# Kernel optimization log

Hardware: AMD Instinct MI355X
Metric: run time of the kernel (lower is better)

Reference implementation:

```python
import jax, jax.numpy as jnp
import numpy as np

N, C, H, M = 4096, 1024, 16, 4096
D = C // H
EPS = 1e-6


def rms_norm(x, g):
    # RMSNorm32: normalize in fp32 with eps=1e-6, affine scale g
    x32 = x.astype(jnp.float32)
    inv = jax.lax.rsqrt(jnp.mean(x32 * x32, axis=-1, keepdims=True) + EPS)
    return (x32 * inv).astype(x.dtype) * g


def setup_inputs() -> dict:
    key = jax.random.key(0)
    ks = jax.random.split(key, 6)
    s = 1.0 / np.sqrt(C)
    return {
        "x": jax.random.normal(ks[0], (N, C), jnp.float32),
        "g1": jnp.ones((C,), jnp.float32),
        "g2": jnp.ones((C,), jnp.float32),
        "w_qkv": jax.random.normal(ks[1], (C, 3 * C), jnp.float32) * s,
        "w_o": jax.random.normal(ks[2], (C, C), jnp.float32) * s,
        "w1": jax.random.normal(ks[3], (C, M), jnp.float32) * s,
        "w2": jax.random.normal(ks[4], (M, C), jnp.float32) * (1.0 / np.sqrt(M)),
    }


def reference(x, g1, g2, w_qkv, w_o, w1, w2):
    # --- pre-norm + full multi-head self-attention over all N sparse tokens ---
    h = rms_norm(x, g1)                                   # [N, C]
    qkv = (h @ w_qkv).reshape(N, 3, H, D)                 # [N, 3, H, D]
    q, k, v = qkv[:, 0], qkv[:, 1], qkv[:, 2]             # [N, H, D]
    scale = 1.0 / np.sqrt(D)
    scores = jnp.einsum('nhd,mhd->hnm', q, k) * scale     # [H, N, N]
    attn = jax.nn.softmax(scores, axis=-1)
    o = jnp.einsum('hnm,mhd->nhd', attn, v).reshape(N, C) # [N, C]
    x = x + o @ w_o                                       # residual
    # --- pre-norm + gated-free MLP (GELU tanh) ---
    h2 = rms_norm(x, g2)
    m = jax.nn.gelu(h2 @ w1, approximate=True) @ w2       # [N, C]
    return x + m
```

## Files before the change

kernel.cpp:

```cpp
#include <hip/hip_runtime.h>
#include <stdint.h>

#define TOK 4096
#define CH  1024
#define NH  16
#define HD  64
#define FF  4096

typedef __attribute__((ext_vector_type(8))) short bf16x8;
typedef __attribute__((ext_vector_type(4))) float f32x4;
typedef __attribute__((ext_vector_type(16))) float f32x16;

__device__ __forceinline__ unsigned short f2bf(float f) {
    union { float f; unsigned u; } v; v.f = f;
    unsigned u = v.u;
    u += 0x7fffu + ((u >> 16) & 1u);
    return (unsigned short)(u >> 16);
}

__device__ __forceinline__ unsigned cvtpk(float a, float b) {
    unsigned r;
    asm("v_cvt_pk_bf16_f32 %0, %1, %2" : "=v"(r) : "v"(a), "v"(b));
    return r;
}

__device__ __forceinline__ void load_lds16(const void* g, void* l) {
    __builtin_amdgcn_global_load_lds(
        (const __attribute__((address_space(1))) unsigned int*)g,
        (__attribute__((address_space(3))) unsigned int*)l, 16, 0, 0);
}

template<int N> __device__ __forceinline__ void wait_vm_lgkm0() {
    if constexpr (N == 0)      asm volatile("s_waitcnt vmcnt(0) lgkmcnt(0)" ::: "memory");
    else if constexpr (N == 4) asm volatile("s_waitcnt vmcnt(4) lgkmcnt(0)" ::: "memory");
    __builtin_amdgcn_sched_barrier(0);
    __builtin_amdgcn_s_barrier();
}

__device__ __forceinline__ float gelu_tanh(float u) {
    float z = 0.7978845608028654f * (u + 0.044715f * u * u * u);
    float e = __expf(2.0f * z);
    return 0.5f * u * (1.0f + (1.0f - 2.0f / (e + 1.0f)));
}

__global__ __launch_bounds__(256) void wT_kernel(const float* __restrict__ in,
                                                 unsigned short* __restrict__ out,
                                                 int K, int Nn) {
    __shared__ float tile[32][33];
    int k0 = blockIdx.x * 32, n0 = blockIdx.y * 32;
    int t = threadIdx.x, r = t >> 3, c = t & 7;
#pragma unroll
    for (int i = 0; i < 4; i++)
        tile[r][c + 8 * i] = in[(size_t)(k0 + r) * Nn + n0 + c + 8 * i];
    __syncthreads();
#pragma unroll
    for (int i = 0; i < 4; i++)
        out[(size_t)(n0 + r) * K + k0 + c + 8 * i] = f2bf(tile[c + 8 * i][r]);
}

__global__ __launch_bounds__(256) void rms_kernel(const float* __restrict__ x,
                                                  const float* __restrict__ g,
                                                  unsigned short* __restrict__ out) {
    int row = blockIdx.x, t = threadIdx.x;
    const float4* xr = (const float4*)(x + (size_t)row * CH);
    float4 v = xr[t];
    float ss = v.x * v.x + v.y * v.y + v.z * v.z + v.w * v.w;
#pragma unroll
    for (int m = 32; m; m >>= 1) ss += __shfl_xor(ss, m, 64);
    __shared__ float wsum[4];
    if ((t & 63) == 0) wsum[t >> 6] = ss;
    __syncthreads();
    float inv = rsqrtf((wsum[0] + wsum[1] + wsum[2] + wsum[3]) * (1.0f / CH) + 1e-6f);
    float4 gv = ((const float4*)g)[t];
    ushort4 o;
    o.x = f2bf(v.x * inv * gv.x);
    o.y = f2bf(v.y * inv * gv.y);
    o.z = f2bf(v.z * inv * gv.z);
    o.w = f2bf(v.w * inv * gv.w);
    ((ushort4*)(out + (size_t)row * CH))[t] = o;
}

template<int BM, int BN, int EPI>
__global__ __launch_bounds__(256) void gemm_bt(const unsigned short* __restrict__ A,
                                               const unsigned short* __restrict__ Bt,
                                               void* __restrict__ outp,
                                               const float* __restrict__ resid,
                                               unsigned short* __restrict__ vout,
                                               int M, int Nn, int K) {
    __shared__ __align__(16) unsigned short ldsA[2][BM * 32];
    __shared__ __align__(16) unsigned short ldsB[2][BN * 32];
    const int t = threadIdx.x, l = t & 63, w = t >> 6;
    const int nbn = Nn / BN;
    const int bid = blockIdx.x, nwg = gridDim.x, cpx = nwg >> 3;
    const int swz = (bid & 7) * cpx + (bid >> 3);
    const int bm = swz / nbn, bn = swz % nbn;
    const int wr = w >> 1, wc = w & 1;
    constexpr int MF = BM / 32, NF = BN / 32;
    const unsigned short* Ag = A + (size_t)bm * BM * K;
    const unsigned short* Bg = Bt + (size_t)bn * BN * K;

    f32x4 acc[MF][NF];
#pragma unroll
    for (int m = 0; m < MF; m++)
#pragma unroll
        for (int n = 0; n < NF; n++) acc[m][n] = {0.f, 0.f, 0.f, 0.f};

    auto stage = [&](int buf, int kt) {
#pragma unroll
        for (int p = 0; p < BM / 64; p++) {
            int c = t + 256 * p;
            load_lds16(Ag + (size_t)(c >> 2) * K + kt * 32 + (c & 3) * 8, &ldsA[buf][c * 8]);
        }
#pragma unroll
        for (int p = 0; p < BN / 64; p++) {
            int c = t + 256 * p;
            load_lds16(Bg + (size_t)(c >> 2) * K + kt * 32 + (c & 3) * 8, &ldsB[buf][c * 8]);
        }
    };

    stage(0, 0);
    __syncthreads();
    const int nkt = K >> 5;
    for (int kt = 0; kt < nkt; kt++) {
        const int buf = kt & 1;
        if (kt + 1 < nkt) stage(buf ^ 1, kt + 1);
        bf16x8 af[MF], bfr[NF];
#pragma unroll
        for (int m = 0; m < MF; m++)
            af[m] = *(const bf16x8*)&ldsA[buf][(wr * (BM / 2) + m * 16 + (l & 15)) * 32 + (l >> 4) * 8];
#pragma unroll
        for (int n = 0; n < NF; n++)
            bfr[n] = *(const bf16x8*)&ldsB[buf][(wc * (BN / 2) + n * 16 + (l & 15)) * 32 + (l >> 4) * 8];
#pragma unroll
        for (int m = 0; m < MF; m++)
#pragma unroll
            for (int n = 0; n < NF; n++)
                acc[m][n] = __builtin_amdgcn_mfma_f32_16x16x32_bf16(af[m], bfr[n], acc[m][n], 0, 0, 0);
        __syncthreads();
    }

    const int r0 = bm * BM + wr * (BM / 2), c0 = bn * BN + wc * (BN / 2);
    const bool vpart = (EPI == 3) && (c0 >= 2048);
#pragma unroll
    for (int m = 0; m < MF; m++)
#pragma unroll
        for (int n = 0; n < NF; n++) {
            if (vpart) {
                int cc = c0 + n * 16 + (l & 15);
                int rrb = r0 + m * 16 + (l >> 4) * 4;
                ushort4 pk;
                pk.x = f2bf(acc[m][n][0]);
                pk.y = f2bf(acc[m][n][1]);
                pk.z = f2bf(acc[m][n][2]);
                pk.w = f2bf(acc[m][n][3]);
                *(ushort4*)(vout + (size_t)(cc - 2048) * 4096 + rrb) = pk;
            } else {
#pragma unroll
                for (int r = 0; r < 4; r++) {
                    int rr = r0 + m * 16 + (l >> 4) * 4 + r;
                    int cc = c0 + n * 16 + (l & 15);
                    float v = acc[m][n][r];
                    if (EPI == 0) {
                        ((unsigned short*)outp)[(size_t)rr * Nn + cc] = f2bf(v);
                    } else if (EPI == 1) {
                        ((unsigned short*)outp)[(size_t)rr * Nn + cc] = f2bf(gelu_tanh(v));
                    } else if (EPI == 3) {
                        float sc = (cc < 1024) ? 0.180336880f : 1.0f;
                        ((unsigned short*)outp)[(size_t)rr * Nn + cc] = f2bf(v * sc);
                    } else {
                        ((float*)outp)[(size_t)rr * Nn + cc] = resid[(size_t)rr * Nn + cc] + v;
                    }
                }
            }
        }
}

__global__ __launch_bounds__(256) void attn_kernel(const unsigned short* __restrict__ qkv,
                                                   const unsigned short* __restrict__ vT,
                                                   unsigned short* __restrict__ o) {
    __shared__ __align__(16) unsigned short Kl[3][4096];
    __shared__ __align__(16) unsigned short Vl[3][4096];
    const int t = threadIdx.x, l = t & 63, w = t >> 6;
    const int h = blockIdx.y;
    const int qrow = blockIdx.x * 128 + w * 32 + (l & 31);

    bf16x8 qf[4];
    {
        const unsigned short* qp = qkv + (size_t)qrow * 3072 + h * 64 + ((l >> 5) * 8);
#pragma unroll
        for (int c = 0; c < 4; c++) qf[c] = *(const bf16x8*)(qp + 16 * c);
    }
    const unsigned short* kb = qkv + 1024 + h * 64;
    const unsigned short* vb = vT + (size_t)h * 64 * 4096;

    int off8[4];
#pragma unroll
    for (int c = 0; c < 4; c++)
        off8[c] = (l & 31) * 64 + ((((l >> 5) + 2 * c) ^ (l & 7)) * 8);
    int kst[2], vst[2];
#pragma unroll
    for (int p = 0; p < 2; p++) {
        int c = t + 256 * p;
        int r = c >> 3, b = c & 7;
        kst[p] = r * 3072 + ((b ^ (r & 7)) * 8);
        vst[p] = r * 4096 + ((b ^ (r & 7)) * 8);
    }

    float lrun = 0.f;
    const f32x16 z16 = {0.f, 0.f, 0.f, 0.f, 0.f, 0.f, 0.f, 0.f,
                        0.f, 0.f, 0.f, 0.f, 0.f, 0.f, 0.f, 0.f};
    f32x16 accO[2];
#pragma unroll
    for (int dt = 0; dt < 2; dt++) accO[dt] = z16;

    auto stage = [&](int buf, int kt) {
#pragma unroll
        for (int p = 0; p < 2; p++)
            load_lds16(kb + (size_t)kt * 64 * 3072 + kst[p], &Kl[buf][(t + 256 * p) * 8]);
#pragma unroll
        for (int p = 0; p < 2; p++)
            load_lds16(vb + kt * 64 + vst[p], &Vl[buf][(t + 256 * p) * 8]);
    };

    stage(0, 0);
    stage(1, 1);
    wait_vm_lgkm0<4>();

    for (int kt = 0; kt < 64; kt++) {
        const int cur = kt % 3;
        if (kt + 2 < 64) stage((kt + 2) % 3, kt + 2);

        f32x16 s[2];
        __builtin_amdgcn_s_setprio(1);
#pragma unroll
        for (int st = 0; st < 2; st++) {
            bf16x8 kf0 = *(const bf16x8*)&Kl[cur][st * 2048 + off8[0]];
            s[st] = __builtin_amdgcn_mfma_f32_32x32x16_bf16(kf0, qf[0], z16, 0, 0, 0);
#pragma unroll
            for (int c = 1; c < 4; c++) {
                bf16x8 kf = *(const bf16x8*)&Kl[cur][st * 2048 + off8[c]];
                s[st] = __builtin_amdgcn_mfma_f32_32x32x16_bf16(kf, qf[c], s[st], 0, 0, 0);
            }
        }
        __builtin_amdgcn_s_setprio(0);

        float rs = 0.f;
#pragma unroll
        for (int st = 0; st < 2; st++)
#pragma unroll
            for (int i = 0; i < 16; i++) {
                float p = __builtin_amdgcn_exp2f(s[st][i]);
                s[st][i] = p;
                rs += p;
            }
        lrun += rs;

#pragma unroll
        for (int kc = 0; kc < 4; kc++) {
            const int base = 8 * (kc & 1);
            const f32x16& S = s[kc >> 1];
            unsigned w0 = cvtpk(S[base + 0], S[base + 1]);
            unsigned w1 = cvtpk(S[base + 2], S[base + 3]);
            unsigned w2 = cvtpk(S[base + 4], S[base + 5]);
            unsigned w3 = cvtpk(S[base + 6], S[base + 7]);
            asm("v_permlane32_swap_b32 %0, %1" : "+v"(w0), "+v"(w2));
            asm("v_permlane32_swap_b32 %0, %1" : "+v"(w1), "+v"(w3));
            union { unsigned u[4]; bf16x8 v; } pf;
            pf.u[0] = w0; pf.u[1] = w1; pf.u[2] = w2; pf.u[3] = w3;
            __builtin_amdgcn_s_setprio(1);
#pragma unroll
            for (int dt = 0; dt < 2; dt++) {
                bf16x8 vf = *(const bf16x8*)&Vl[cur][dt * 2048 + off8[kc]];
                accO[dt] = __builtin_amdgcn_mfma_f32_32x32x16_bf16(vf, pf.v, accO[dt], 0, 0, 0);
            }
            __builtin_amdgcn_s_setprio(0);
        }

        if (kt < 63) {
            if (kt + 2 < 64) wait_vm_lgkm0<4>();
            else             wait_vm_lgkm0<0>();
        }
    }

    lrun += __shfl_xor(lrun, 32, 64);
    float inv = 1.0f / lrun;
    unsigned short* ob = o + (size_t)qrow * CH + h * 64 + 4 * (l >> 5);
#pragma unroll
    for (int dt = 0; dt < 2; dt++)
#pragma unroll
        for (int qd = 0; qd < 4; qd++) {
            ushort4 pk;
            pk.x = f2bf(accO[dt][qd * 4 + 0] * inv);
            pk.y = f2bf(accO[dt][qd * 4 + 1] * inv);
            pk.z = f2bf(accO[dt][qd * 4 + 2] * inv);
            pk.w = f2bf(accO[dt][qd * 4 + 3] * inv);
            *(ushort4*)(ob + dt * 32 + qd * 8) = pk;
        }
}

extern "C" void kernel_launch(void* const* d_in, const int* in_sizes, int n_in,
                              void* d_out, int out_size, void* d_ws, size_t ws_size,
                              hipStream_t stream) {
    const float* x     = (const float*)d_in[0];
    const float* g1    = (const float*)d_in[1];
    const float* g2    = (const float*)d_in[2];
    const float* w_qkv = (const float*)d_in[3];
    const float* w_o   = (const float*)d_in[4];
    const float* w1    = (const float*)d_in[5];
    const float* w2    = (const float*)d_in[6];

    char* ws = (char*)d_ws;
    unsigned short* wqkvT = (unsigned short*)(ws);
    unsigned short* woT   = (unsigned short*)(ws + 6291456);
    unsigned short* w1T   = (unsigned short*)(ws + 8388608);
    unsigned short* w2T   = (unsigned short*)(ws + 16777216);
    unsigned short* hbuf  = (unsigned short*)(ws + 25165824);
    unsigned short* qkv   = (unsigned short*)(ws + 33554432);
    unsigned short* obuf  = (unsigned short*)(ws + 58720256);
    float*          x2    = (float*)(ws + 67108864);
    unsigned short* abuf  = (unsigned short*)(ws + 83886080);
    unsigned short* vTb   = (unsigned short*)(ws + 83886080);

    dim3 b256(256);
    wT_kernel<<<dim3(CH / 32, 3 * CH / 32), b256, 0, stream>>>(w_qkv, wqkvT, CH, 3 * CH);
    wT_kernel<<<dim3(CH / 32, CH / 32),     b256, 0, stream>>>(w_o,   woT,   CH, CH);
    wT_kernel<<<dim3(CH / 32, FF / 32),     b256, 0, stream>>>(w1,    w1T,   CH, FF);
    wT_kernel<<<dim3(FF / 32, CH / 32),     b256, 0, stream>>>(w2,    w2T,   FF, CH);

    rms_kernel<<<TOK, b256, 0, stream>>>(x, g1, hbuf);
    gemm_bt<128, 128, 3><<<(TOK / 128) * (3 * CH / 128), b256, 0, stream>>>(hbuf, wqkvT, qkv, nullptr, vTb, TOK, 3 * CH, CH);
    attn_kernel<<<dim3(TOK / 128, NH), b256, 0, stream>>>(qkv, vTb, obuf);
    gemm_bt<64, 64, 2><<<(TOK / 64) * (CH / 64), b256, 0, stream>>>(obuf, woT, x2, x, nullptr, TOK, CH, CH);
    rms_kernel<<<TOK, b256, 0, stream>>>(x2, g2, hbuf);
    gemm_bt<128, 128, 1><<<(TOK / 128) * (FF / 128), b256, 0, stream>>>(hbuf, w1T, abuf, nullptr, nullptr, TOK, FF, CH);
    gemm_bt<64, 64, 2><<<(TOK / 64) * (CH / 64), b256, 0, stream>>>(abuf, w2T, (float*)d_out, x2, nullptr, TOK, CH, FF);
}
```

Before: 305.8 us.

## Software-pipeline attention loop with 4-deep K/V buffers and QK lookahead

Restructures the attention main loop so the QK^T MFMAs for the next key tile are issued before the softmax and PV work of the current tile, using two alternating score register sets. K/V LDS staging grows from triple to quadruple buffering, prefetching three tiles ahead with adjusted vmcnt waits. The goal is to hide exp/convert latency and load latency behind matrix work. In exchange it raises LDS use per block to 64KB, which may lower the number of resident blocks, and it increases register pressure.

After: 307.5 us. No clear change (+0.6%).

```diff
diff --git a/kernel.cpp b/kernel.cpp
--- a/kernel.cpp
+++ b/kernel.cpp
@@ -33,6 +33,7 @@
 template<int N> __device__ __forceinline__ void wait_vm_lgkm0() {
     if constexpr (N == 0)      asm volatile("s_waitcnt vmcnt(0) lgkmcnt(0)" ::: "memory");
     else if constexpr (N == 4) asm volatile("s_waitcnt vmcnt(4) lgkmcnt(0)" ::: "memory");
+    else if constexpr (N == 8) asm volatile("s_waitcnt vmcnt(8) lgkmcnt(0)" ::: "memory");
     __builtin_amdgcn_sched_barrier(0);
     __builtin_amdgcn_s_barrier();
 }
@@ -178,8 +179,8 @@
 __global__ __launch_bounds__(256) void attn_kernel(const unsigned short* __restrict__ qkv,
                                                    const unsigned short* __restrict__ vT,
                                                    unsigned short* __restrict__ o) {
-    __shared__ __align__(16) unsigned short Kl[3][4096];
-    __shared__ __align__(16) unsigned short Vl[3][4096];
+    __shared__ __align__(16) unsigned short Kl[4][4096];
+    __shared__ __align__(16) unsigned short Vl[4][4096];
     const int t = threadIdx.x, l = t & 63, w = t >> 6;
     const int h = blockIdx.y;
     const int qrow = blockIdx.x * 128 + w * 32 + (l & 31);
@@ -213,37 +214,33 @@
 #pragma unroll
     for (int dt = 0; dt < 2; dt++) accO[dt] = z16;
 
-    auto stage = [&](int buf, int kt) {
+    auto stage = [&](int tile) {
+        const int buf = tile & 3;
 #pragma unroll
         for (int p = 0; p < 2; p++)
-            load_lds16(kb + (size_t)kt * 64 * 3072 + kst[p], &Kl[buf][(t + 256 * p) * 8]);
+            load_lds16(kb + (size_t)tile * 64 * 3072 + kst[p], &Kl[buf][(t + 256 * p) * 8]);
 #pragma unroll
         for (int p = 0; p < 2; p++)
-            load_lds16(vb + kt * 64 + vst[p], &Vl[buf][(t + 256 * p) * 8]);
+            load_lds16(vb + tile * 64 + vst[p], &Vl[buf][(t + 256 * p) * 8]);
     };
 
-    stage(0, 0);
-    stage(1, 1);
-    wait_vm_lgkm0<4>();
-
-    for (int kt = 0; kt < 64; kt++) {
-        const int cur = kt % 3;
-        if (kt + 2 < 64) stage((kt + 2) % 3, kt + 2);
-
-        f32x16 s[2];
+    auto qk = [&](int tile, f32x16* s) {
+        const unsigned short* kl = &Kl[tile & 3][0];
         __builtin_amdgcn_s_setprio(1);
 #pragma unroll
         for (int st = 0; st < 2; st++) {
-            bf16x8 kf0 = *(const bf16x8*)&Kl[cur][st * 2048 + off8[0]];
+            bf16x8 kf0 = *(const bf16x8*)&kl[st * 2048 + off8[0]];
             s[st] = __builtin_amdgcn_mfma_f32_32x32x16_bf16(kf0, qf[0], z16, 0, 0, 0);
 #pragma unroll
             for (int c = 1; c < 4; c++) {
-                bf16x8 kf = *(const bf16x8*)&Kl[cur][st * 2048 + off8[c]];
+                bf16x8 kf = *(const bf16x8*)&kl[st * 2048 + off8[c]];
                 s[st] = __builtin_amdgcn_mfma_f32_32x32x16_bf16(kf, qf[c], s[st], 0, 0, 0);
             }
         }
         __builtin_amdgcn_s_setprio(0);
-
+    };
+
+    auto smpv = [&](int tile, f32x16* s) {
         float rs = 0.f;
 #pragma unroll
         for (int st = 0; st < 2; st++)
@@ -254,7 +251,7 @@
                 rs += p;
             }
         lrun += rs;
-
+        const unsigned short* vl = &Vl[tile & 3][0];
 #pragma unroll
         for (int kc = 0; kc < 4; kc++) {
             const int base = 8 * (kc & 1);
@@ -270,15 +267,33 @@
             __builtin_amdgcn_s_setprio(1);
 #pragma unroll
             for (int dt = 0; dt < 2; dt++) {
-                bf16x8 vf = *(const bf16x8*)&Vl[cur][dt * 2048 + off8[kc]];
+                bf16x8 vf = *(const bf16x8*)&vl[dt * 2048 + off8[kc]];
                 accO[dt] = __builtin_amdgcn_mfma_f32_32x32x16_bf16(vf, pf.v, accO[dt], 0, 0, 0);
             }
             __builtin_amdgcn_s_setprio(0);
         }
-
-        if (kt < 63) {
-            if (kt + 2 < 64) wait_vm_lgkm0<4>();
-            else             wait_vm_lgkm0<0>();
+    };
+
+    f32x16 sA[2], sB[2];
+
+    stage(0); stage(1); stage(2);
+    wait_vm_lgkm0<8>();
+    qk(0, sA);
+
+    for (int j = 0; j < 64; j += 2) {
+        if (j <= 60) wait_vm_lgkm0<4>();
+        else         wait_vm_lgkm0<0>();
+        if (j + 3 < 64) stage(j + 3);
+        qk(j + 1, sB);
+        smpv(j, sA);
+        const int jo = j + 1;
+        if (jo < 63) {
+            wait_vm_lgkm0<4>();
+            if (jo + 3 < 64) stage(jo + 3);
+            qk(jo + 1, sA);
+            smpv(jo, sB);
+        } else {
+            smpv(63, sB);
         }
     }
 
```

## Add 256x256-tile 512-thread GEMM for QKV and FC1 projections

Applied to the files above, without the earlier changes.

Introduces a new gemm256 kernel with 256x256 output tiles, 8 waves, 64-wide K steps, XOR-swizzled LDS layout, quarter-step staging interleaved with MFMA compute, and s_setprio around the MFMA bursts. The QKV projection (with its V-transpose epilogue) and the FC1+GELU projection now use it instead of the 128x128 gemm_bt. The aim is higher arithmetic intensity per LDS byte and better overlap of global-to-LDS loads with compute. In exchange it uses more registers and LDS, and it launches fewer workgroups (192 and 256), which may leave the GPU's CUs under-occupied.

New measurement: 293.7 us. -4.0%, faster.

```diff
diff --git a/kernel.cpp b/kernel.cpp
--- a/kernel.cpp
+++ b/kernel.cpp
@@ -33,6 +33,7 @@
 template<int N> __device__ __forceinline__ void wait_vm_lgkm0() {
     if constexpr (N == 0)      asm volatile("s_waitcnt vmcnt(0) lgkmcnt(0)" ::: "memory");
     else if constexpr (N == 4) asm volatile("s_waitcnt vmcnt(4) lgkmcnt(0)" ::: "memory");
+    else if constexpr (N == 8) asm volatile("s_waitcnt vmcnt(8) lgkmcnt(0)" ::: "memory");
     __builtin_amdgcn_sched_barrier(0);
     __builtin_amdgcn_s_barrier();
 }
@@ -85,7 +86,6 @@
                                                const unsigned short* __restrict__ Bt,
                                                void* __restrict__ outp,
                                                const float* __restrict__ resid,
-                                               unsigned short* __restrict__ vout,
                                                int M, int Nn, int K) {
     __shared__ __align__(16) unsigned short ldsA[2][BM * 32];
     __shared__ __align__(16) unsigned short ldsB[2][BN * 32];
@@ -140,11 +140,113 @@
     }
 
     const int r0 = bm * BM + wr * (BM / 2), c0 = bn * BN + wc * (BN / 2);
+#pragma unroll
+    for (int m = 0; m < MF; m++)
+#pragma unroll
+        for (int n = 0; n < NF; n++)
+#pragma unroll
+            for (int r = 0; r < 4; r++) {
+                int rr = r0 + m * 16 + (l >> 4) * 4 + r;
+                int cc = c0 + n * 16 + (l & 15);
+                float v = acc[m][n][r];
+                if (EPI == 0) {
+                    ((unsigned short*)outp)[(size_t)rr * Nn + cc] = f2bf(v);
+                } else if (EPI == 1) {
+                    ((unsigned short*)outp)[(size_t)rr * Nn + cc] = f2bf(gelu_tanh(v));
+                } else {
+                    ((float*)outp)[(size_t)rr * Nn + cc] = resid[(size_t)rr * Nn + cc] + v;
+                }
+            }
+}
+
+template<int EPI>
+__global__ __launch_bounds__(512) void gemm256(const unsigned short* __restrict__ A,
+                                               const unsigned short* __restrict__ Bt,
+                                               void* __restrict__ outp,
+                                               unsigned short* __restrict__ vout,
+                                               int M, int Nn, int K) {
+    __shared__ __align__(16) unsigned short lds[2][4][8192];
+    const int t = threadIdx.x, l = t & 63, w = t >> 6;
+    const int wr = w >> 2, wc = w & 3;
+    const int nbn = Nn >> 8;
+    const int bid = blockIdx.x, nwg = gridDim.x, cpx = nwg >> 3;
+    const int swz = (bid & 7) * cpx + (bid >> 3);
+    const int bm = swz / nbn, bn = swz % nbn;
+
+    const int lbase = (((l & 15) * 64 + (l >> 4) * 16)) ^ (((l >> 3) & 1) << 5);
+
+    int srow[2], scol[2];
+#pragma unroll
+    for (int L = 0; L < 2; L++) {
+        int g = t + L * 512;
+        int s = g >> 6;
+        int wb = ((g & 63) * 16) ^ (((g >> 5) & 1) << 5);
+        srow[L] = (s >> 1) * 16 + (wb >> 6);
+        scol[L] = (s & 1) * 32 + ((wb & 63) >> 1);
+    }
+
+    const unsigned short* Asrc = A + (size_t)(bm * 256) * K;
+    const unsigned short* Bsrc = Bt + (size_t)(bn * 256) * K;
+
+    auto stage_half = [&](int j) {
+        const int kt = j >> 2, slot = j & 3;
+        const unsigned short* base = (slot < 2 ? Asrc : Bsrc) + (size_t)((slot & 1) * 128) * K;
+#pragma unroll
+        for (int L = 0; L < 2; L++)
+            load_lds16(base + (size_t)srow[L] * K + kt * 64 + scol[L],
+                       &lds[kt & 1][slot][(t + L * 512) * 8]);
+    };
+
+    f32x4 acc[8][4];
+#pragma unroll
+    for (int m = 0; m < 8; m++)
+#pragma unroll
+        for (int n = 0; n < 4; n++) acc[m][n] = {0.f, 0.f, 0.f, 0.f};
+
+    const int nkt = K >> 6;
+    stage_half(0); stage_half(1); stage_half(2); stage_half(3);
+
+    for (int kt = 0; kt < nkt; kt++) {
+        wait_vm_lgkm0<0>();
+        const char* Abase = (const char*)&lds[kt & 1][wr][0];
+        const char* Bbase = (const char*)&lds[kt & 1][2 + (wc >> 1)][0];
+        bf16x8 bfr[4][2];
+#pragma unroll
+        for (int q = 0; q < 4; q++) {
+            if (q == 0) {
+#pragma unroll
+                for (int n = 0; n < 4; n++)
+#pragma unroll
+                    for (int ks = 0; ks < 2; ks++)
+                        bfr[n][ks] = *(const bf16x8*)(Bbase + ((((wc & 1) * 4 + n) * 2 + ks) * 1024 + lbase));
+            }
+            bf16x8 af[2][2];
+#pragma unroll
+            for (int mi = 0; mi < 2; mi++)
+#pragma unroll
+                for (int ks = 0; ks < 2; ks++)
+                    af[mi][ks] = *(const bf16x8*)(Abase + (((q * 2 + mi) * 2 + ks) * 1024 + lbase));
+            if (kt + 1 < nkt) stage_half((kt + 1) * 4 + q);
+            __builtin_amdgcn_s_barrier();
+            __builtin_amdgcn_s_setprio(1);
+#pragma unroll
+            for (int mi = 0; mi < 2; mi++)
+#pragma unroll
+                for (int n = 0; n < 4; n++) {
+                    acc[q * 2 + mi][n] = __builtin_amdgcn_mfma_f32_16x16x32_bf16(af[mi][0], bfr[n][0], acc[q * 2 + mi][n], 0, 0, 0);
+                    acc[q * 2 + mi][n] = __builtin_amdgcn_mfma_f32_16x16x32_bf16(af[mi][1], bfr[n][1], acc[q * 2 + mi][n], 0, 0, 0);
+                }
+            __builtin_amdgcn_s_setprio(0);
+            __builtin_amdgcn_s_barrier();
+        }
+    }
+
+    const int r0 = bm * 256 + wr * 128, c0 = bn * 256 + wc * 64;
     const bool vpart = (EPI == 3) && (c0 >= 2048);
 #pragma unroll
-    for (int m = 0; m < MF; m++)
-#pragma unroll
-        for (int n = 0; n < NF; n++) {
+    for (int m = 0; m < 8; m++)
+#pragma unroll
+        for (int n = 0; n < 4; n++) {
             if (vpart) {
                 int cc = c0 + n * 16 + (l & 15);
                 int rrb = r0 + m * 16 + (l >> 4) * 4;
@@ -160,15 +262,11 @@
                     int rr = r0 + m * 16 + (l >> 4) * 4 + r;
                     int cc = c0 + n * 16 + (l & 15);
                     float v = acc[m][n][r];
-                    if (EPI == 0) {
-                        ((unsigned short*)outp)[(size_t)rr * Nn + cc] = f2bf(v);
-                    } else if (EPI == 1) {
+                    if (EPI == 1) {
                         ((unsigned short*)outp)[(size_t)rr * Nn + cc] = f2bf(gelu_tanh(v));
-                    } else if (EPI == 3) {
+                    } else {
                         float sc = (cc < 1024) ? 0.180336880f : 1.0f;
                         ((unsigned short*)outp)[(size_t)rr * Nn + cc] = f2bf(v * sc);
-                    } else {
-                        ((float*)outp)[(size_t)rr * Nn + cc] = resid[(size_t)rr * Nn + cc] + v;
                     }
                 }
             }
@@ -321,17 +419,17 @@
     unsigned short* abuf  = (unsigned short*)(ws + 83886080);
     unsigned short* vTb   = (unsigned short*)(ws + 83886080);
 
-    dim3 b256(256);
+    dim3 b256(256), b512(512);
     wT_kernel<<<dim3(CH / 32, 3 * CH / 32), b256, 0, stream>>>(w_qkv, wqkvT, CH, 3 * CH);
     wT_kernel<<<dim3(CH / 32, CH / 32),     b256, 0, stream>>>(w_o,   woT,   CH, CH);
     wT_kernel<<<dim3(CH / 32, FF / 32),     b256, 0, stream>>>(w1,    w1T,   CH, FF);
     wT_kernel<<<dim3(FF / 32, CH / 32),     b256, 0, stream>>>(w2,    w2T,   FF, CH);
 
     rms_kernel<<<TOK, b256, 0, stream>>>(x, g1, hbuf);
-    gemm_bt<128, 128, 3><<<(TOK / 128) * (3 * CH / 128), b256, 0, stream>>>(hbuf, wqkvT, qkv, nullptr, vTb, TOK, 3 * CH, CH);
+    gemm256<3><<<(TOK / 256) * (3 * CH / 256), b512, 0, stream>>>(hbuf, wqkvT, qkv, vTb, TOK, 3 * CH, CH);
     attn_kernel<<<dim3(TOK / 128, NH), b256, 0, stream>>>(qkv, vTb, obuf);
-    gemm_bt<64, 64, 2><<<(TOK / 64) * (CH / 64), b256, 0, stream>>>(obuf, woT, x2, x, nullptr, TOK, CH, CH);
+    gemm_bt<64, 64, 2><<<(TOK / 64) * (CH / 64), b256, 0, stream>>>(obuf, woT, x2, x, TOK, CH, CH);
     rms_kernel<<<TOK, b256, 0, stream>>>(x2, g2, hbuf);
-    gemm_bt<128, 128, 1><<<(TOK / 128) * (FF / 128), b256, 0, stream>>>(hbuf, w1T, abuf, nullptr, nullptr, TOK, FF, CH);
-    gemm_bt<64, 64, 2><<<(TOK / 64) * (CH / 64), b256, 0, stream>>>(abuf, w2T, (float*)d_out, x2, nullptr, TOK, CH, FF);
-}
+    gemm256<1><<<(TOK / 256) * (FF / 256), b512, 0, stream>>>(hbuf, w1T, abuf, nullptr, TOK, FF, CH);
+    gemm_bt<64, 64, 2><<<(TOK / 64) * (CH / 64), b256, 0, stream>>>(abuf, w2T, (float*)d_out, x2, TOK, CH, FF);
+}
```
